# Optimization experiments

Measured on AMD Instinct MI355X. Metric: run time of the kernel, lower is better.

Reference implementation:

```python
import jax, jax.numpy as jnp
import numpy as np

B, DIM, N = 64, 128, 4000
H = 4
DH = DIM // H          # 32
CL = 50                # clusters (hardcoded in module)
K = 9                  # knn_num
SCALOR = DH ** -0.5


def setup_inputs() -> dict:
    key = jax.random.key(0)
    ks = jax.random.split(key, 16)
    s = 0.05
    inp = {
        'x': jax.random.normal(ks[0], (B, DIM, N, 1), jnp.float32),
        # conv_group1 / conv_group2: InstanceNorm(no affine) -> BN(affine) -> ReLU -> 1x1 conv
        'wg1': jax.random.normal(ks[1], (CL, DIM), jnp.float32) * s,
        'bg1': jnp.zeros((CL,), jnp.float32),
        'g1_gamma': jnp.ones((DIM,), jnp.float32),
        'g1_beta': jnp.zeros((DIM,), jnp.float32),
        'wg2': jax.random.normal(ks[2], (CL, DIM), jnp.float32) * s,
        'bg2': jnp.zeros((CL,), jnp.float32),
        'g2_gamma': jnp.ones((DIM,), jnp.float32),
        'g2_beta': jnp.zeros((DIM,), jnp.float32),
        # per-head 1x1 convs (stacked over heads)
        'qkv_w': jax.random.normal(ks[3], (H, DH, DIM), jnp.float32) * s,
        'qkv_b': jnp.zeros((H, DH), jnp.float32),
        'qkv1_w': jax.random.normal(ks[4], (H, 3 * DH, DIM), jnp.float32) * s,
        'qkv1_b': jnp.zeros((H, 3 * DH), jnp.float32),
        # GCBlock convs: conv1 (1,3) stride (1,3): 2*DH->DH ; conv2 (1,3): DH->DH
        'gc1_w': jax.random.normal(ks[5], (H, DH, 2 * DH, 3), jnp.float32) * s,
        'gc1_b': jnp.zeros((H, DH), jnp.float32),
        'gc1_gamma': jnp.ones((H, DH), jnp.float32),
        'gc1_beta': jnp.zeros((H, DH), jnp.float32),
        'gc2_w': jax.random.normal(ks[6], (H, DH, DH, 3), jnp.float32) * s,
        'gc2_b': jnp.zeros((H, DH), jnp.float32),
        'gc2_gamma': jnp.ones((H, DH), jnp.float32),
        'gc2_beta': jnp.zeros((H, DH), jnp.float32),
        # output projections
        'pres_w': jax.random.normal(ks[7], (DIM, 2 * DIM), jnp.float32) * s,
        'pres_b': jnp.zeros((DIM,), jnp.float32),
        'proj_w': jax.random.normal(ks[8], (DIM, DIM), jnp.float32) * s,
        'proj_b': jnp.zeros((DIM,), jnp.float32),
    }
    return inp


def _conv_group(x3, w, bconv, gamma, beta):
    # x3: (b, C, n). InstanceNorm2d(eps=1e-3, no affine) over n, BN(train) over (b,n), ReLU, 1x1 conv.
    mu = x3.mean(-1, keepdims=True)
    var = x3.var(-1, keepdims=True)
    xin = (x3 - mu) * jax.lax.rsqrt(var + 1e-3)
    mu2 = xin.mean((0, 2), keepdims=True)
    var2 = xin.var((0, 2), keepdims=True)
    xbn = gamma[None, :, None] * (xin - mu2) * jax.lax.rsqrt(var2 + 1e-5) + beta[None, :, None]
    xr = jax.nn.relu(xbn)
    return jnp.einsum('oc,bcn->bon', w, xr) + bconv[None, :, None]


def _bn_train(h, gamma, beta, axes):
    mu = h.mean(axes, keepdims=True)
    var = h.var(axes, keepdims=True)
    return gamma * (h - mu) * jax.lax.rsqrt(var + 1e-5) + beta


def _forward(x, wg1, bg1, g1_gamma, g1_beta, wg2, bg2, g2_gamma, g2_beta,
             qkv_w, qkv_b, qkv1_w, qkv1_b,
             gc1_w, gc1_b, gc1_gamma, gc1_beta,
             gc2_w, gc2_b, gc2_gamma, gc2_beta,
             pres_w, pres_b, proj_w, proj_b):
    xs = x[..., 0]                                          # (b, dim, n)
    # cluster assignment 1: softmax over points
    embed1 = _conv_group(xs, wg1, bg1, g1_gamma, g1_beta)   # (b, 50, n)
    S1 = jax.nn.softmax(embed1, axis=2)
    cluster_x = jnp.einsum('bdn,bcn->bdc', xs, S1)          # (b, dim, 50)

    # ---- local branch (per head, vectorized): 1x1 conv -> knn graph feature -> conv stack ----
    q = jnp.einsum('hod,bdc->bhoc', qkv_w, cluster_x) + qkv_b[None, :, :, None]  # (b,H,dh,50)
    xt = q.transpose(0, 1, 3, 2)                            # (b,H,50,dh)
    inner = jnp.einsum('bhnc,bhmc->bhnm', xt, xt)
    sq = jnp.sum(xt * xt, axis=-1)
    pd = 2.0 * inner - sq[..., :, None] - sq[..., None, :]  # negative squared distance
    idx = jax.lax.top_k(pd, K)[1]                            # (b,H,50,K)
    x_exp = jnp.broadcast_to(xt[:, :, None, :, :], xt.shape[:2] + (CL, CL, DH))
    feature = jnp.take_along_axis(x_exp, idx[..., None], axis=3)        # (b,H,50,K,dh)
    center = jnp.broadcast_to(xt[:, :, :, None, :], feature.shape)
    edge = jnp.concatenate([center, center - feature], axis=-1)          # (b,H,50,K,2dh)
    # conv1: kernel (1,3) stride (1,3): K=9 -> 3 windows of 3
    e = edge.reshape(edge.shape[0], H, CL, 3, 3, 2 * DH)
    h1 = jnp.einsum('bhnjti,hoit->bhnjo', e, gc1_w) + gc1_b[None, :, None, None, :]
    h1 = jax.nn.relu(_bn_train(h1, gc1_gamma[None, :, None, None, :], gc1_beta[None, :, None, None, :], (0, 2, 3)))
    # conv2: kernel (1,3): 3 -> 1
    h2 = jnp.einsum('bhnti,hoit->bhno', h1, gc2_w) + gc2_b[None, :, None, :]
    h2 = jax.nn.relu(_bn_train(h2, gc2_gamma[None, :, None, :], gc2_beta[None, :, None, :], (0, 2)))
    local = h2.transpose(0, 1, 3, 2)                        # (b,H,dh,50)

    # ---- global branch: tiny attention over 50 clusters per head ----
    qkv = jnp.einsum('hod,bdc->bhoc', qkv1_w, cluster_x) + qkv1_b[None, :, :, None]  # (b,H,3dh,50)
    qg, kg, vg = jnp.split(qkv, 3, axis=2)
    attn = jax.nn.softmax(SCALOR * jnp.einsum('bhdn,bhdm->bhnm', qg, kg), axis=-1)
    glob = jnp.einsum('bhnm,bhdm->bhdn', attn, vg)          # (b,H,dh,50)

    # interleave [local_h, global_h] per head along channels -> (b, 2*dim, 50)
    per_head = jnp.concatenate([local, glob], axis=2)       # (b,H,2dh,50)
    cat = per_head.reshape(per_head.shape[0], 2 * DIM, CL)
    res = jnp.einsum('oc,bcn->bon', pres_w, cat) + pres_b[None, :, None]  # (b,dim,50)

    # cluster assignment 2: softmax over clusters, scatter back to points
    embed2 = _conv_group(xs, wg2, bg2, g2_gamma, g2_beta)   # (b,50,n)
    S2 = jax.nn.softmax(embed2, axis=1)
    res2 = jnp.einsum('bdc,bcn->bdn', res, S2)              # (b,dim,n)
    out = jnp.einsum('od,bdn->bon', proj_w, res2) + proj_b[None, :, None]
    return out[..., None]                                   # (b,dim,n,1)


def reference(x, wg1, bg1, g1_gamma, g1_beta, wg2, bg2, g2_gamma, g2_beta,
              qkv_w, qkv_b, qkv1_w, qkv1_b,
              gc1_w, gc1_b, gc1_gamma, gc1_beta,
              gc2_w, gc2_b, gc2_gamma, gc2_beta,
              pres_w, pres_b, proj_w, proj_b):
    return _forward(x, wg1, bg1, g1_gamma, g1_beta, wg2, bg2, g2_gamma, g2_beta,
                    qkv_w, qkv_b, qkv1_w, qkv1_b,
                    gc1_w, gc1_b, gc1_gamma, gc1_beta,
                    gc2_w, gc2_b, gc2_gamma, gc2_beta,
                    pres_w, pres_b, proj_w, proj_b)
```

## Files before the change

### kernel.cpp

```cpp
#include <hip/hip_runtime.h>
#include <cstddef>


constexpr size_t O_MU    = 0;
constexpr size_t O_RINV  = 8192;
constexpr size_t O_RATIO = 16384;
constexpr size_t O_A1    = 24576;
constexpr size_t O_B1    = 24704;
constexpr size_t O_A2    = 24832;
constexpr size_t O_B2    = 24960;
constexpr size_t O_PROJWT= 25088;
constexpr size_t O_VPROJ = 41472;
constexpr size_t O_MT    = 41600;
constexpr size_t O_E2    = 74368;
constexpr size_t O_UCXP  = 12874368;
constexpr size_t O_CX    = 16659072;
constexpr size_t O_XT    = 17068672;
constexpr size_t O_QT    = 17478272;
constexpr size_t O_KT    = 17887872;
constexpr size_t O_VT    = 18297472;
constexpr size_t O_H1    = 18707072;
constexpr size_t O_P1    = 19935872;
constexpr size_t O_BN1S  = 19952256;
constexpr size_t O_BN1T  = 19952384;
constexpr size_t O_H2    = 19952512;
constexpr size_t O_P2    = 20362112;
constexpr size_t O_BN2S  = 20378496;
constexpr size_t O_BN2T  = 20378624;
constexpr size_t O_CAT   = 20378752;
constexpr size_t O_PRES2 = 21197952;

__global__ __launch_bounds__(256) void k_rowstats(const float* __restrict__ x,
                                                  float* __restrict__ ws){
  int row = blockIdx.x;
  const float4* xr = (const float4*)(x + (size_t)row * 4000);
  float s = 0.f, sq = 0.f;
  for(int i = threadIdx.x; i < 1000; i += 256){
    float4 v = xr[i];
    s  += v.x + v.y + v.z + v.w;
    sq += v.x*v.x + v.y*v.y + v.z*v.z + v.w*v.w;
  }
  __shared__ float ls[256], lq[256];
  ls[threadIdx.x] = s; lq[threadIdx.x] = sq; __syncthreads();
  for(int st = 128; st > 0; st >>= 1){
    if(threadIdx.x < st){ ls[threadIdx.x] += ls[threadIdx.x+st]; lq[threadIdx.x] += lq[threadIdx.x+st]; }
    __syncthreads();
  }
  if(threadIdx.x == 0){
    float mean = ls[0] * (1.f/4000.f);
    float var  = lq[0] * (1.f/4000.f) - mean*mean;
    ws[O_MU   + row] = mean;
    ws[O_RINV + row] = rsqrtf(var + 1e-3f);
    ws[O_RATIO+ row] = var / (var + 1e-3f);
  }
}

__global__ void k_prep(const float* g1g, const float* g1b,
                       const float* g2g, const float* g2b,
                       const float* presb, const float* projw,
                       float* __restrict__ ws){
  int t = threadIdx.x;
  if(t < 128){
    float s = 0.f;
    for(int b = 0; b < 64; b++) s += ws[O_RATIO + b*128 + t];
    float var2 = s * (1.f/64.f);
    float inv2 = rsqrtf(var2 + 1e-5f);
    ws[O_A1+t] = g1g[t] * inv2;  ws[O_B1+t] = g1b[t];
    ws[O_A2+t] = g2g[t] * inv2;  ws[O_B2+t] = g2b[t];
  }
  for(int i = t; i < 16384; i += 256){ int o = i & 127, k = i >> 7; ws[O_PROJWT+i] = projw[o*128 + k]; }
  __syncthreads();
  if(t < 128){
    float v = 0.f;
    for(int d = 0; d < 128; d++) v += ws[O_PROJWT + d*128 + t] * presb[d];
    ws[O_VPROJ + t] = v;
  }
}

__global__ __launch_bounds__(256) void k_mprep(const float* __restrict__ presw,
                                               float* __restrict__ ws){
  int kk2 = blockIdx.x * 2;
  __shared__ float pwc[2][128];
  int t = threadIdx.x;
  { int which = t >> 7, d = t & 127; pwc[which][d] = presw[d*256 + kk2 + which]; }
  __syncthreads();
  int which = t >> 7, o = t & 127;
  float acc = 0.f;
  for(int d = 0; d < 128; d++) acc += ws[O_PROJWT + d*128 + o] * pwc[which][d];
  ws[O_MT + (size_t)(kk2 + which)*128 + o] = acc;
}

__global__ __launch_bounds__(256) void k_fused(const float* __restrict__ x,
    const float* __restrict__ wg1, const float* __restrict__ bg1,
    const float* __restrict__ wg2, const float* __restrict__ bg2,
    float* __restrict__ ws){
  int ch = blockIdx.x, b = blockIdx.y;
  __shared__ float lW1[128*56];
  __shared__ float lW2[128*56];
  __shared__ float lrv1[128*64];
  __shared__ float lrv2[128*64];
  __shared__ float lxt [64*132];
  __shared__ float ca1[128], cb1[128], ca2[128], cb2[128];
  __shared__ float bg1p[64], bg2p[64];
  int t = threadIdx.x;
  if(t < 128){
    float mu = ws[O_MU + b*128 + t], ri = ws[O_RINV + b*128 + t];
    float a1 = ws[O_A1+t]*ri, a2 = ws[O_A2+t]*ri;
    ca1[t] = a1; cb1[t] = ws[O_B1+t] - a1*mu;
    ca2[t] = a2; cb2[t] = ws[O_B2+t] - a2*mu;
  }
  if(t < 64){ bg1p[t] = (t < 50) ? bg1[t] : 0.f; bg2p[t] = (t < 50) ? bg2[t] : 0.f; }
  for(int i = t; i < 1600; i += 256){
    int cl = i >> 5, cq = i & 31;
    float4 w1 = *(const float4*)&wg1[cl*128 + cq*4];
    float4 w2 = *(const float4*)&wg2[cl*128 + cq*4];
    int c0 = cq*4;
    lW1[(c0+0)*56+cl] = w1.x; lW1[(c0+1)*56+cl] = w1.y; lW1[(c0+2)*56+cl] = w1.z; lW1[(c0+3)*56+cl] = w1.w;
    lW2[(c0+0)*56+cl] = w2.x; lW2[(c0+1)*56+cl] = w2.y; lW2[(c0+2)*56+cl] = w2.z; lW2[(c0+3)*56+cl] = w2.w;
  }
  for(int i = t; i < 768; i += 256){
    int cl = 50 + i/128, c = i%128;
    lW1[c*56+cl] = 0.f; lW2[c*56+cl] = 0.f;
  }
  int dg = t % 33, cg = t / 33;
  float ua[4][8];
  #pragma unroll
  for(int r = 0; r < 4; r++)
    #pragma unroll
    for(int i = 0; i < 8; i++) ua[r][i] = 0.f;
  int ig = t >> 4, jg = t & 15;
  int clb = ig*4, j4 = jg*4;
  float e[4][4];

  for(int st = 0; st < 8; st++){
    int nb = ch*500 + st*64;
    int lim = (st == 7) ? 52 : 64;
    __syncthreads();
    for(int i = t; i < 2048; i += 256){
      int c = i >> 4, jj = (i & 15)*4;
      float4 xv = make_float4(0.f,0.f,0.f,0.f);
      if(jj < lim) xv = *(const float4*)&x[(size_t)(b*128 + c)*4000 + nb + jj];
      lxt[(jj+0)*132 + c] = xv.x; lxt[(jj+1)*132 + c] = xv.y;
      lxt[(jj+2)*132 + c] = xv.z; lxt[(jj+3)*132 + c] = xv.w;
      float a1 = ca1[c], b1v = cb1[c], a2 = ca2[c], b2v = cb2[c];
      float4 r1, r2;
      r1.x = fmaxf(a1*xv.x + b1v, 0.f); r1.y = fmaxf(a1*xv.y + b1v, 0.f);
      r1.z = fmaxf(a1*xv.z + b1v, 0.f); r1.w = fmaxf(a1*xv.w + b1v, 0.f);
      r2.x = fmaxf(a2*xv.x + b2v, 0.f); r2.y = fmaxf(a2*xv.y + b2v, 0.f);
      r2.z = fmaxf(a2*xv.z + b2v, 0.f); r2.w = fmaxf(a2*xv.w + b2v, 0.f);
      *(float4*)&lrv1[c*64 + jj] = r1;
      *(float4*)&lrv2[c*64 + jj] = r2;
    }
    if(t < 64){
      lxt[t*132 + 128] = (t < lim) ? 1.f : 0.f;
      lxt[t*132 + 129] = 0.f; lxt[t*132 + 130] = 0.f; lxt[t*132 + 131] = 0.f;
    }
    __syncthreads();
    if(ig < 14){
      #pragma unroll
      for(int r = 0; r < 4; r++){ e[r][0]=0.f; e[r][1]=0.f; e[r][2]=0.f; e[r][3]=0.f; }
      #pragma unroll 4
      for(int c = 0; c < 128; c++){
        float4 w = *(const float4*)&lW1[c*56 + clb];
        float4 v = *(const float4*)&lrv1[c*64 + j4];
        e[0][0] += w.x*v.x; e[0][1] += w.x*v.y; e[0][2] += w.x*v.z; e[0][3] += w.x*v.w;
        e[1][0] += w.y*v.x; e[1][1] += w.y*v.y; e[1][2] += w.y*v.z; e[1][3] += w.y*v.w;
        e[2][0] += w.z*v.x; e[2][1] += w.z*v.y; e[2][2] += w.z*v.z; e[2][3] += w.z*v.w;
        e[3][0] += w.w*v.x; e[3][1] += w.w*v.y; e[3][2] += w.w*v.z; e[3][3] += w.w*v.w;
      }
    }
    __syncthreads();
    if(ig < 14){
      #pragma unroll
      for(int r = 0; r < 4; r++){
        float bias = bg1p[clb + r];
        float4 u;
        u.x = expf(e[r][0] + bias); u.y = expf(e[r][1] + bias);
        u.z = expf(e[r][2] + bias); u.w = expf(e[r][3] + bias);
        *(float4*)&lrv1[(clb + r)*64 + j4] = u;
      }
    }
    __syncthreads();
    if(t < 231){
      int d4 = dg*4, cb8 = cg*8;
      #pragma unroll 2
      for(int n = 0; n < 64; n++){
        float4 xv = *(const float4*)&lxt[n*132 + d4];
        #pragma unroll
        for(int i = 0; i < 8; i++){
          float u = lrv1[(cb8 + i)*64 + n];
          ua[0][i] += xv.x*u; ua[1][i] += xv.y*u;
          ua[2][i] += xv.z*u; ua[3][i] += xv.w*u;
        }
      }
    }
    if(ig < 14){
      #pragma unroll
      for(int r = 0; r < 4; r++){ e[r][0]=0.f; e[r][1]=0.f; e[r][2]=0.f; e[r][3]=0.f; }
      #pragma unroll 4
      for(int c = 0; c < 128; c++){
        float4 w = *(const float4*)&lW2[c*56 + clb];
        float4 v = *(const float4*)&lrv2[c*64 + j4];
        e[0][0] += w.x*v.x; e[0][1] += w.x*v.y; e[0][2] += w.x*v.z; e[0][3] += w.x*v.w;
        e[1][0] += w.y*v.x; e[1][1] += w.y*v.y; e[1][2] += w.y*v.z; e[1][3] += w.y*v.w;
        e[2][0] += w.z*v.x; e[2][1] += w.z*v.y; e[2][2] += w.z*v.z; e[2][3] += w.z*v.w;
        e[3][0] += w.w*v.x; e[3][1] += w.w*v.y; e[3][2] += w.w*v.z; e[3][3] += w.w*v.w;
      }
      if(j4 < lim){
        #pragma unroll
        for(int r = 0; r < 4; r++){
          int cl = clb + r;
          if(cl < 50){
            float bias = bg2p[cl];
            float4 o = make_float4(e[r][0]+bias, e[r][1]+bias, e[r][2]+bias, e[r][3]+bias);
            *(float4*)&ws[O_E2 + ((size_t)b*50 + cl)*4000 + nb + j4] = o;
          }
        }
      }
    }
  }
  if(t < 231){
    int d4 = dg*4, cb8 = cg*8;
    #pragma unroll
    for(int r = 0; r < 4; r++){
      size_t base = O_UCXP + ((size_t)(ch*64 + b)*132 + d4 + r)*56 + cb8;
      *(float4*)&ws[base]     = make_float4(ua[r][0], ua[r][1], ua[r][2], ua[r][3]);
      *(float4*)&ws[base + 4] = make_float4(ua[r][4], ua[r][5], ua[r][6], ua[r][7]);
    }
  }
}

__global__ __launch_bounds__(256) void k_cxred(float* __restrict__ ws){
  int b = blockIdx.x, t = threadIdx.x;
  __shared__ float zi[64];
  if(t < 50){
    float s = 0.f;
    for(int ch = 0; ch < 8; ch++)
      s += ws[O_UCXP + ((size_t)(ch*64 + b)*132 + 128)*56 + t];
    zi[t] = 1.f / s;
  }
  __syncthreads();
  for(int i = t; i < 6400; i += 256){
    int d = i / 50, c = i % 50;
    float s = 0.f;
    for(int ch = 0; ch < 8; ch++)
      s += ws[O_UCXP + ((size_t)(ch*64 + b)*132 + d)*56 + c];
    ws[O_CX + (size_t)b*6400 + d*50 + c] = s * zi[c];
  }
}

__global__ __launch_bounds__(256) void k_qkv(const float* __restrict__ qw,
                                             const float* __restrict__ qb,
                                             const float* __restrict__ q1w,
                                             const float* __restrict__ q1b,
                                             float* __restrict__ ws){
  int rt = blockIdx.x, b = blockIdx.y;
  __shared__ float wl[64*130];
  __shared__ float cxl[128*52];
  int t = threadIdx.x;
  for(int i = t; i < 2048; i += 256){
    int rl = i >> 5, kq = i & 31, row = rt*64 + rl;
    float4 w = (row < 128) ? *(const float4*)&qw[row*128 + kq*4]
                           : *(const float4*)&q1w[(row-128)*128 + kq*4];
    int k0 = kq*4;
    wl[rl*130 + k0+0] = w.x; wl[rl*130 + k0+1] = w.y;
    wl[rl*130 + k0+2] = w.z; wl[rl*130 + k0+3] = w.w;
  }
  for(int i = t; i < 6656; i += 256){
    int k = i / 52, c = i % 52;
    cxl[i] = (c < 50) ? ws[O_CX + (size_t)b*6400 + k*50 + c] : 0.f;
  }
  __syncthreads();
  int ig = t & 15, cg = t >> 4;
  float acc[4][4];
  #pragma unroll
  for(int r = 0; r < 4; r++){ acc[r][0]=0.f; acc[r][1]=0.f; acc[r][2]=0.f; acc[r][3]=0.f; }
  if(cg < 13){
    int rb = ig*4, cb = cg*4;
    #pragma unroll 4
    for(int k = 0; k < 128; k++){
      float4 cv = *(const float4*)&cxl[k*52 + cb];
      float w0 = wl[(rb+0)*130 + k], w1 = wl[(rb+1)*130 + k];
      float w2 = wl[(rb+2)*130 + k], w3 = wl[(rb+3)*130 + k];
      acc[0][0] += w0*cv.x; acc[0][1] += w0*cv.y; acc[0][2] += w0*cv.z; acc[0][3] += w0*cv.w;
      acc[1][0] += w1*cv.x; acc[1][1] += w1*cv.y; acc[1][2] += w1*cv.z; acc[1][3] += w1*cv.w;
      acc[2][0] += w2*cv.x; acc[2][1] += w2*cv.y; acc[2][2] += w2*cv.z; acc[2][3] += w2*cv.w;
      acc[3][0] += w3*cv.x; acc[3][1] += w3*cv.y; acc[3][2] += w3*cv.z; acc[3][3] += w3*cv.w;
    }
    #pragma unroll
    for(int r = 0; r < 4; r++){
      int row = rt*64 + ig*4 + r;
      size_t base; float bias;
      if(row < 128){
        int h = row >> 5;
        bias = qb[row];
        base = O_XT + (size_t)(b*4 + h)*1600 + (row & 31);
      }else{
        int r2 = row - 128, h = r2/96, j = r2%96, kind = j >> 5, dd = j & 31;
        bias = q1b[r2];
        base = (kind==0 ? O_QT : kind==1 ? O_KT : O_VT) + (size_t)(b*4 + h)*1600 + dd;
      }
      #pragma unroll
      for(int s = 0; s < 4; s++){
        int c = cg*4 + s;
        if(c < 50) ws[base + (size_t)c*32] = acc[r][s] + bias;
      }
    }
  }
}

__global__ __launch_bounds__(256) void k_knn(const float* __restrict__ g1w,
                                             const float* __restrict__ g1bias,
                                             float* __restrict__ ws){
  int h = blockIdx.x, b = blockIdx.y;
  __shared__ float xtl[50][33];
  __shared__ float pdl[50][52];
  __shared__ float sql[50];
  __shared__ int   idxl[50][9];
  __shared__ float w1l[6144];
  int t = threadIdx.x;
  const float* xtg = ws + O_XT + (size_t)(b*4 + h)*1600;
  for(int i = t; i < 1600; i += 256) xtl[i >> 5][i & 31] = xtg[i];
  for(int i = t; i < 6144; i += 256){
    int o = i / 192, r = i % 192, ii = r / 3, tt = r % 3;
    w1l[(ii*3 + tt)*32 + o] = g1w[(size_t)h*6144 + i];
  }
  __syncthreads();
  if(t < 50){
    float s = 0.f;
    for(int d = 0; d < 32; d++){ float v = xtl[t][d]; s += v*v; }
    sql[t] = s;
  }
  __syncthreads();
  for(int i = t; i < 2500; i += 256){
    int n = i / 50, m = i % 50;
    float s = 0.f;
    for(int d = 0; d < 32; d++) s += xtl[n][d]*xtl[m][d];
    pdl[n][m] = 2.f*s - sql[n] - sql[m];
  }
  __syncthreads();
  if(t < 50){
    float pv = INFINITY; int pi = -1;
    for(int k = 0; k < 9; k++){
      float bv = -INFINITY; int bi = 1000;
      for(int m = 0; m < 50; m++){
        float v = pdl[t][m];
        bool elig = (v < pv) || (v == pv && m > pi);
        if(elig && (v > bv || (v == bv && m < bi))){ bv = v; bi = m; }
      }
      idxl[t][k] = bi; pv = bv; pi = bi;
    }
  }
  __syncthreads();
  if(t < 150){
    int n = t / 3, jw = t % 3;
    float acc[32];
    #pragma unroll
    for(int o = 0; o < 32; o++) acc[o] = 0.f;
    for(int t3 = 0; t3 < 3; t3++){
      int kx = idxl[n][jw*3 + t3];
      for(int ii = 0; ii < 32; ii++){
        float c0 = xtl[n][ii];
        float c1 = c0 - xtl[kx][ii];
        const float* wr0 = w1l + (ii*3 + t3)*32;
        const float* wr1 = w1l + ((ii+32)*3 + t3)*32;
        #pragma unroll
        for(int o = 0; o < 32; o++) acc[o] += c0*wr0[o] + c1*wr1[o];
      }
    }
    float* out = ws + O_H1 + ((size_t)(b*4 + h)*150 + n*3 + jw)*32;
    #pragma unroll
    for(int o = 0; o < 32; o++) out[o] = acc[o] + g1bias[h*32 + o];
  }
}

__global__ void k_bn1p(float* __restrict__ ws){
  int b = blockIdx.x, t = threadIdx.x;
  int p = t & 127, half = t >> 7;
  int h = p >> 5, o = p & 31;
  const float* src = ws + O_H1 + (size_t)b*19200;
  float s = 0.f, sq = 0.f;
  for(int nj = half*75; nj < half*75 + 75; nj++){
    float v = src[(h*150 + nj)*32 + o];
    s += v; sq += v*v;
  }
  __shared__ float ls[256], lq[256];
  ls[t] = s; lq[t] = sq; __syncthreads();
  if(t < 128){
    ws[O_P1 + b*256 + p]       = ls[t] + ls[t+128];
    ws[O_P1 + b*256 + 128 + p] = lq[t] + lq[t+128];
  }
}

__global__ void k_bn1f(const float* g, const float* be, float* __restrict__ ws){
  int t = threadIdx.x;
  if(t < 128){
    float s = 0.f, sq = 0.f;
    for(int b = 0; b < 64; b++){ s += ws[O_P1 + b*256 + t]; sq += ws[O_P1 + b*256 + 128 + t]; }
    float mean = s * (1.f/9600.f), var = sq * (1.f/9600.f) - mean*mean;
    float sc = g[t] * rsqrtf(var + 1e-5f);
    ws[O_BN1S+t] = sc; ws[O_BN1T+t] = be[t] - sc*mean;
  }
}

__global__ __launch_bounds__(256) void k_conv2(const float* __restrict__ g2w,
                                               const float* __restrict__ g2bias,
                                               float* __restrict__ ws){
  int h = blockIdx.x, b = blockIdx.y;
  __shared__ float hl[150][33];
  __shared__ float w2l[3072];
  __shared__ float rs[8][32], rq[8][32];
  int t = threadIdx.x;
  const float* h1p = ws + O_H1 + (size_t)(b*4 + h)*4800;
  for(int i = t; i < 4800; i += 256){
    int nj = i >> 5, ii = i & 31;
    hl[nj][ii] = fmaxf(ws[O_BN1S + h*32 + ii]*h1p[i] + ws[O_BN1T + h*32 + ii], 0.f);
  }
  for(int i = t; i < 3072; i += 256){
    int o = i / 96, r = i % 96, ii = r / 3, tt = r % 3;
    w2l[(ii*3 + tt)*32 + o] = g2w[(size_t)h*3072 + i];
  }
  __syncthreads();
  int o = t & 31, ng = t >> 5;
  float bias = g2bias[h*32 + o];
  float s = 0.f, sq = 0.f;
  for(int n = ng; n < 50; n += 8){
    float acc = 0.f;
    for(int t3 = 0; t3 < 3; t3++){
      const float* hr = hl[n*3 + t3];
      #pragma unroll
      for(int ii = 0; ii < 32; ii++) acc += hr[ii] * w2l[(ii*3 + t3)*32 + o];
    }
    acc += bias;
    ws[O_H2 + ((size_t)(b*4 + h)*50 + n)*32 + o] = acc;
    s += acc; sq += acc*acc;
  }
  rs[ng][o] = s; rq[ng][o] = sq; __syncthreads();
  if(t < 32){
    float S = 0.f, Q = 0.f;
    for(int g2 = 0; g2 < 8; g2++){ S += rs[g2][t]; Q += rq[g2][t]; }
    ws[O_P2 + (b*4 + h)*64 + t]      = S;
    ws[O_P2 + (b*4 + h)*64 + 32 + t] = Q;
  }
}

__global__ void k_bn2f(const float* g, const float* be, float* __restrict__ ws){
  int t = threadIdx.x;
  if(t < 128){
    int h = t >> 5, o = t & 31;
    float s = 0.f, sq = 0.f;
    for(int b = 0; b < 64; b++){
      s  += ws[O_P2 + (size_t)(b*4 + h)*64 + o];
      sq += ws[O_P2 + (size_t)(b*4 + h)*64 + 32 + o];
    }
    float mean = s * (1.f/3200.f), var = sq * (1.f/3200.f) - mean*mean;
    float sc = g[t] * rsqrtf(var + 1e-5f);
    ws[O_BN2S+t] = sc; ws[O_BN2T+t] = be[t] - sc*mean;
  }
}

__global__ __launch_bounds__(256) void k_attn(float* __restrict__ ws){
  int h = blockIdx.x, b = blockIdx.y;
  __shared__ float qtl[50][33], ktl[50][33], vtl[50][33], al[50][52];
  int t = threadIdx.x;
  size_t base = (size_t)(b*4 + h)*1600;
  for(int i = t; i < 1600; i += 256){
    int n = i >> 5, d = i & 31;
    qtl[n][d] = ws[O_QT + base + i];
    ktl[n][d] = ws[O_KT + base + i];
    vtl[n][d] = ws[O_VT + base + i];
  }
  __syncthreads();
  for(int i = t; i < 2500; i += 256){
    int n = i / 50, m = i % 50;
    float s = 0.f;
    for(int d = 0; d < 32; d++) s += qtl[n][d]*ktl[m][d];
    al[n][m] = s * 0.17677669529663687f;
  }
  __syncthreads();
  if(t < 50){
    float m = -INFINITY;
    for(int j = 0; j < 50; j++) m = fmaxf(m, al[t][j]);
    float s = 0.f;
    for(int j = 0; j < 50; j++){ float e = expf(al[t][j] - m); al[t][j] = e; s += e; }
    float inv = 1.f/s;
    for(int j = 0; j < 50; j++) al[t][j] *= inv;
  }
  __syncthreads();
  for(int i = t; i < 1600; i += 256){
    int n = i >> 5, d = i & 31;
    float gacc = 0.f;
    for(int m = 0; m < 50; m++) gacc += al[n][m]*vtl[m][d];
    ws[O_CAT + ((size_t)b*256 + h*64 + 32 + d)*50 + n] = gacc;
    float l = fmaxf(ws[O_BN2S + h*32 + d]*ws[O_H2 + ((size_t)(b*4 + h)*50 + n)*32 + d] + ws[O_BN2T + h*32 + d], 0.f);
    ws[O_CAT + ((size_t)b*256 + h*64 + d)*50 + n] = l;
  }
}

__global__ __launch_bounds__(256) void k_res(float* __restrict__ ws){
  int b = blockIdx.x;
  __shared__ float mtl[64*132];
  __shared__ float catl[64*52];
  __shared__ float vp[128];
  int t = threadIdx.x;
  if(t < 128) vp[t] = ws[O_VPROJ + t];
  int og = t >> 4, cg = t & 15;
  int ob = og*8, cb = cg*4;
  float acc[8][4];
  #pragma unroll
  for(int r = 0; r < 8; r++){ acc[r][0]=0.f; acc[r][1]=0.f; acc[r][2]=0.f; acc[r][3]=0.f; }
  for(int kc = 0; kc < 4; kc++){
    int k0 = kc*64;
    __syncthreads();
    for(int i = t; i < 2048; i += 256){
      int k = i >> 5, oq = i & 31;
      float4 m = *(const float4*)&ws[O_MT + (size_t)(k0 + k)*128 + oq*4];
      *(float4*)&mtl[k*132 + oq*4] = m;
    }
    for(int i = t; i < 3328; i += 256){
      int k = i / 52, c = i % 52;
      catl[i] = (c < 50) ? ws[O_CAT + (size_t)b*12800 + (k0 + k)*50 + c] : 0.f;
    }
    __syncthreads();
    if(cg < 13){
      #pragma unroll 2
      for(int k = 0; k < 64; k++){
        float4 m0 = *(const float4*)&mtl[k*132 + ob];
        float4 m1 = *(const float4*)&mtl[k*132 + ob + 4];
        float4 cv = *(const float4*)&catl[k*52 + cb];
        acc[0][0] += m0.x*cv.x; acc[0][1] += m0.x*cv.y; acc[0][2] += m0.x*cv.z; acc[0][3] += m0.x*cv.w;
        acc[1][0] += m0.y*cv.x; acc[1][1] += m0.y*cv.y; acc[1][2] += m0.y*cv.z; acc[1][3] += m0.y*cv.w;
        acc[2][0] += m0.z*cv.x; acc[2][1] += m0.z*cv.y; acc[2][2] += m0.z*cv.z; acc[2][3] += m0.z*cv.w;
        acc[3][0] += m0.w*cv.x; acc[3][1] += m0.w*cv.y; acc[3][2] += m0.w*cv.z; acc[3][3] += m0.w*cv.w;
        acc[4][0] += m1.x*cv.x; acc[4][1] += m1.x*cv.y; acc[4][2] += m1.x*cv.z; acc[4][3] += m1.x*cv.w;
        acc[5][0] += m1.y*cv.x; acc[5][1] += m1.y*cv.y; acc[5][2] += m1.y*cv.z; acc[5][3] += m1.y*cv.w;
        acc[6][0] += m1.z*cv.x; acc[6][1] += m1.z*cv.y; acc[6][2] += m1.z*cv.z; acc[6][3] += m1.z*cv.w;
        acc[7][0] += m1.w*cv.x; acc[7][1] += m1.w*cv.y; acc[7][2] += m1.w*cv.z; acc[7][3] += m1.w*cv.w;
      }
    }
  }
  if(cg < 13){
    #pragma unroll
    for(int s = 0; s < 4; s++){
      int c = cb + s;
      if(c < 50){
        float4 o0 = make_float4(acc[0][s]+vp[ob+0], acc[1][s]+vp[ob+1], acc[2][s]+vp[ob+2], acc[3][s]+vp[ob+3]);
        float4 o1 = make_float4(acc[4][s]+vp[ob+4], acc[5][s]+vp[ob+5], acc[6][s]+vp[ob+6], acc[7][s]+vp[ob+7]);
        *(float4*)&ws[O_PRES2 + (size_t)b*6400 + c*128 + ob]     = o0;
        *(float4*)&ws[O_PRES2 + (size_t)b*6400 + c*128 + ob + 4] = o1;
      }
    }
  }
}

__global__ __launch_bounds__(256) void k_out(const float* __restrict__ projb,
                                             float* __restrict__ ws,
                                             float* __restrict__ out){
  int nt = blockIdx.x, b = blockIdx.y;
  int n0 = nt*64;
  __shared__ float sl[50*64];
  __shared__ float p2l[50*132];
  __shared__ float pb[128];
  int t = threadIdx.x;
  for(int i = t; i < 3200; i += 256){
    int c = i >> 6, j = i & 63, n = n0 + j;
    sl[i] = (n < 4000) ? ws[O_E2 + ((size_t)b*50 + c)*4000 + n] : 0.f;
  }
  for(int i = t; i < 6400; i += 256){
    int c = i >> 7, o = i & 127;
    p2l[c*132 + o] = ws[O_PRES2 + (size_t)b*6400 + c*128 + o];
  }
  if(t < 128) pb[t] = projb[t];
  __syncthreads();
  if(t < 64){
    int j = t;
    float m = -INFINITY;
    for(int c = 0; c < 50; c++) m = fmaxf(m, sl[c*64 + j]);
    float s = 0.f;
    for(int c = 0; c < 50; c++){ float e = expf(sl[c*64 + j] - m); sl[c*64 + j] = e; s += e; }
    float inv = 1.f/s;
    for(int c = 0; c < 50; c++) sl[c*64 + j] *= inv;
  }
  __syncthreads();
  int og = t >> 4, jg = t & 15;
  int ob = og*8, j4 = jg*4;
  float acc[8][4];
  #pragma unroll
  for(int r = 0; r < 8; r++){ acc[r][0]=0.f; acc[r][1]=0.f; acc[r][2]=0.f; acc[r][3]=0.f; }
  #pragma unroll 2
  for(int c = 0; c < 50; c++){
    float4 sv = *(const float4*)&sl[c*64 + j4];
    float4 p0 = *(const float4*)&p2l[c*132 + ob];
    float4 p1 = *(const float4*)&p2l[c*132 + ob + 4];
    acc[0][0] += p0.x*sv.x; acc[0][1] += p0.x*sv.y; acc[0][2] += p0.x*sv.z; acc[0][3] += p0.x*sv.w;
    acc[1][0] += p0.y*sv.x; acc[1][1] += p0.y*sv.y; acc[1][2] += p0.y*sv.z; acc[1][3] += p0.y*sv.w;
    acc[2][0] += p0.z*sv.x; acc[2][1] += p0.z*sv.y; acc[2][2] += p0.z*sv.z; acc[2][3] += p0.z*sv.w;
    acc[3][0] += p0.w*sv.x; acc[3][1] += p0.w*sv.y; acc[3][2] += p0.w*sv.z; acc[3][3] += p0.w*sv.w;
    acc[4][0] += p1.x*sv.x; acc[4][1] += p1.x*sv.y; acc[4][2] += p1.x*sv.z; acc[4][3] += p1.x*sv.w;
    acc[5][0] += p1.y*sv.x; acc[5][1] += p1.y*sv.y; acc[5][2] += p1.y*sv.z; acc[5][3] += p1.y*sv.w;
    acc[6][0] += p1.z*sv.x; acc[6][1] += p1.z*sv.y; acc[6][2] += p1.z*sv.z; acc[6][3] += p1.z*sv.w;
    acc[7][0] += p1.w*sv.x; acc[7][1] += p1.w*sv.y; acc[7][2] += p1.w*sv.z; acc[7][3] += p1.w*sv.w;
  }
  int n = n0 + j4;
  if(n < 4000){
    #pragma unroll
    for(int r = 0; r < 8; r++){
      float bv = pb[ob + r];
      float4 o = make_float4(acc[r][0]+bv, acc[r][1]+bv, acc[r][2]+bv, acc[r][3]+bv);
      *(float4*)&out[(size_t)(b*128 + ob + r)*4000 + n] = o;
    }
  }
}

extern "C" void kernel_launch(void* const* d_in, const int* in_sizes, int n_in,
                              void* d_out, int out_size, void* d_ws, size_t ws_size,
                              hipStream_t stream){
  (void)in_sizes; (void)n_in; (void)out_size; (void)ws_size;
  const float* x      = (const float*)d_in[0];
  const float* wg1    = (const float*)d_in[1];
  const float* bg1    = (const float*)d_in[2];
  const float* g1g    = (const float*)d_in[3];
  const float* g1b    = (const float*)d_in[4];
  const float* wg2    = (const float*)d_in[5];
  const float* bg2    = (const float*)d_in[6];
  const float* g2g    = (const float*)d_in[7];
  const float* g2b    = (const float*)d_in[8];
  const float* qkvw   = (const float*)d_in[9];
  const float* qkvb   = (const float*)d_in[10];
  const float* qkv1w  = (const float*)d_in[11];
  const float* qkv1b  = (const float*)d_in[12];
  const float* gc1w   = (const float*)d_in[13];
  const float* gc1bias= (const float*)d_in[14];
  const float* gc1g   = (const float*)d_in[15];
  const float* gc1be  = (const float*)d_in[16];
  const float* gc2w   = (const float*)d_in[17];
  const float* gc2bias= (const float*)d_in[18];
  const float* gc2g   = (const float*)d_in[19];
  const float* gc2be  = (const float*)d_in[20];
  const float* presw  = (const float*)d_in[21];
  const float* presb  = (const float*)d_in[22];
  const float* projw  = (const float*)d_in[23];
  const float* projb  = (const float*)d_in[24];
  float* ws = (float*)d_ws;
  float* out = (float*)d_out;

  k_rowstats<<<8192, 256, 0, stream>>>(x, ws);
  k_prep<<<1, 256, 0, stream>>>(g1g, g1b, g2g, g2b, presb, projw, ws);
  k_mprep<<<128, 256, 0, stream>>>(presw, ws);
  k_fused<<<dim3(8, 64), 256, 0, stream>>>(x, wg1, bg1, wg2, bg2, ws);
  k_cxred<<<64, 256, 0, stream>>>(ws);
  k_qkv<<<dim3(8, 64), 256, 0, stream>>>(qkvw, qkvb, qkv1w, qkv1b, ws);
  k_knn<<<dim3(4, 64), 256, 0, stream>>>(gc1w, gc1bias, ws);
  k_bn1p<<<64, 256, 0, stream>>>(ws);
  k_bn1f<<<1, 128, 0, stream>>>(gc1g, gc1be, ws);
  k_conv2<<<dim3(4, 64), 256, 0, stream>>>(gc2w, gc2bias, ws);
  k_bn2f<<<1, 128, 0, stream>>>(gc2g, gc2be, ws);
  k_attn<<<dim3(4, 64), 256, 0, stream>>>(ws);
  k_res<<<64, 256, 0, stream>>>(ws);
  k_out<<<dim3(63, 64), 256, 0, stream>>>(projb, ws, out);
}
```

Baseline: 865.6 us.

## Split fused cluster-embedding kernel into separate E1/UCX and E2 kernels

Splits the single fused kernel, which computed both cluster embeddings and the x·u accumulation, into two kernels. Each now uses far less shared memory, so more blocks can be resident per CU. The E1 kernel uses 48-point tiles and computes the softmax normaliser with an explicit row sum instead of the constant-one column trick. It also reorganises the accumulation loop with float4 loads of u. The cost is reading x twice from global memory and one extra kernel launch.

```diff
diff --git a/kernel.cpp b/kernel.cpp
--- a/kernel.cpp
+++ b/kernel.cpp
@@ -90,48 +90,172 @@
   ws[O_MT + (size_t)(kk2 + which)*128 + o] = acc;
 }
 
-__global__ __launch_bounds__(256) void k_fused(const float* __restrict__ x,
+__global__ __launch_bounds__(256) void k_e1ucx(const float* __restrict__ x,
     const float* __restrict__ wg1, const float* __restrict__ bg1,
-    const float* __restrict__ wg2, const float* __restrict__ bg2,
     float* __restrict__ ws){
   int ch = blockIdx.x, b = blockIdx.y;
-  __shared__ float lW1[128*56];
-  __shared__ float lW2[128*56];
-  __shared__ float lrv1[128*64];
-  __shared__ float lrv2[128*64];
-  __shared__ float lxt [64*132];
-  __shared__ float ca1[128], cb1[128], ca2[128], cb2[128];
-  __shared__ float bg1p[64], bg2p[64];
+  __shared__ float lW1[128*52];
+  __shared__ float lrv1[128*48];
+  __shared__ float lxt [48*132];
+  __shared__ float ca1[128], cb1[128];
+  __shared__ float bg1p[56];
   int t = threadIdx.x;
   if(t < 128){
     float mu = ws[O_MU + b*128 + t], ri = ws[O_RINV + b*128 + t];
-    float a1 = ws[O_A1+t]*ri, a2 = ws[O_A2+t]*ri;
+    float a1 = ws[O_A1+t]*ri;
     ca1[t] = a1; cb1[t] = ws[O_B1+t] - a1*mu;
-    ca2[t] = a2; cb2[t] = ws[O_B2+t] - a2*mu;
-  }
-  if(t < 64){ bg1p[t] = (t < 50) ? bg1[t] : 0.f; bg2p[t] = (t < 50) ? bg2[t] : 0.f; }
-  for(int i = t; i < 1600; i += 256){
+  }
+  if(t < 56) bg1p[t] = (t < 50) ? bg1[t] : 0.f;
+  for(int i = t; i < 1664; i += 256){
     int cl = i >> 5, cq = i & 31;
-    float4 w1 = *(const float4*)&wg1[cl*128 + cq*4];
-    float4 w2 = *(const float4*)&wg2[cl*128 + cq*4];
+    float4 w = (cl < 50) ? *(const float4*)&wg1[cl*128 + cq*4] : make_float4(0.f,0.f,0.f,0.f);
     int c0 = cq*4;
-    lW1[(c0+0)*56+cl] = w1.x; lW1[(c0+1)*56+cl] = w1.y; lW1[(c0+2)*56+cl] = w1.z; lW1[(c0+3)*56+cl] = w1.w;
-    lW2[(c0+0)*56+cl] = w2.x; lW2[(c0+1)*56+cl] = w2.y; lW2[(c0+2)*56+cl] = w2.z; lW2[(c0+3)*56+cl] = w2.w;
-  }
-  for(int i = t; i < 768; i += 256){
-    int cl = 50 + i/128, c = i%128;
-    lW1[c*56+cl] = 0.f; lW2[c*56+cl] = 0.f;
-  }
-  int dg = t % 33, cg = t / 33;
+    lW1[(c0+0)*52+cl] = w.x; lW1[(c0+1)*52+cl] = w.y;
+    lW1[(c0+2)*52+cl] = w.z; lW1[(c0+3)*52+cl] = w.w;
+  }
+  int dg = t & 31, cg = t >> 5;
   float ua[4][8];
   #pragma unroll
   for(int r = 0; r < 4; r++)
     #pragma unroll
     for(int i = 0; i < 8; i++) ua[r][i] = 0.f;
+  float zacc = 0.f;
   int ig = t >> 4, jg = t & 15;
   int clb = ig*4, j4 = jg*4;
-  float e[4][4];
-
+
+  for(int st = 0; st < 11; st++){
+    int nb = ch*500 + st*48;
+    int lim = (st == 10) ? 20 : 48;
+    __syncthreads();
+    for(int i = t; i < 1536; i += 256){
+      int c = i / 12, jj = (i % 12)*4;
+      float4 xv = make_float4(0.f,0.f,0.f,0.f);
+      if(jj < lim) xv = *(const float4*)&x[(size_t)(b*128 + c)*4000 + nb + jj];
+      lxt[(jj+0)*132 + c] = xv.x; lxt[(jj+1)*132 + c] = xv.y;
+      lxt[(jj+2)*132 + c] = xv.z; lxt[(jj+3)*132 + c] = xv.w;
+      float a1 = ca1[c], b1v = cb1[c];
+      float4 r1;
+      r1.x = fmaxf(a1*xv.x + b1v, 0.f); r1.y = fmaxf(a1*xv.y + b1v, 0.f);
+      r1.z = fmaxf(a1*xv.z + b1v, 0.f); r1.w = fmaxf(a1*xv.w + b1v, 0.f);
+      *(float4*)&lrv1[c*48 + jj] = r1;
+    }
+    __syncthreads();
+    float e[4][4];
+    if(ig < 13 && jg < 12){
+      #pragma unroll
+      for(int r = 0; r < 4; r++){ e[r][0]=0.f; e[r][1]=0.f; e[r][2]=0.f; e[r][3]=0.f; }
+      #pragma unroll 4
+      for(int c = 0; c < 128; c++){
+        float4 w = *(const float4*)&lW1[c*52 + clb];
+        float4 v = *(const float4*)&lrv1[c*48 + j4];
+        e[0][0] += w.x*v.x; e[0][1] += w.x*v.y; e[0][2] += w.x*v.z; e[0][3] += w.x*v.w;
+        e[1][0] += w.y*v.x; e[1][1] += w.y*v.y; e[1][2] += w.y*v.z; e[1][3] += w.y*v.w;
+        e[2][0] += w.z*v.x; e[2][1] += w.z*v.y; e[2][2] += w.z*v.z; e[2][3] += w.z*v.w;
+        e[3][0] += w.w*v.x; e[3][1] += w.w*v.y; e[3][2] += w.w*v.z; e[3][3] += w.w*v.w;
+      }
+    }
+    __syncthreads();
+    if(ig < 13 && jg < 12){
+      bool live = (j4 < lim);
+      #pragma unroll
+      for(int r = 0; r < 4; r++){
+        float bias = bg1p[clb + r];
+        float4 u = make_float4(0.f,0.f,0.f,0.f);
+        if(live){
+          u.x = expf(e[r][0] + bias); u.y = expf(e[r][1] + bias);
+          u.z = expf(e[r][2] + bias); u.w = expf(e[r][3] + bias);
+        }
+        *(float4*)&lrv1[(clb + r)*48 + j4] = u;
+      }
+    }
+    __syncthreads();
+    if(t < 224){
+      int d4 = dg*4, c8 = cg*8;
+      for(int n4 = 0; n4 < 12; n4++){
+        int n0 = n4*4;
+        float4 uv[8];
+        #pragma unroll
+        for(int i = 0; i < 8; i++) uv[i] = *(const float4*)&lrv1[(c8 + i)*48 + n0];
+        {
+          float4 xq = *(const float4*)&lxt[(n0+0)*132 + d4];
+          #pragma unroll
+          for(int i = 0; i < 8; i++){
+            float u = uv[i].x;
+            ua[0][i] += xq.x*u; ua[1][i] += xq.y*u; ua[2][i] += xq.z*u; ua[3][i] += xq.w*u;
+          }
+        }
+        {
+          float4 xq = *(const float4*)&lxt[(n0+1)*132 + d4];
+          #pragma unroll
+          for(int i = 0; i < 8; i++){
+            float u = uv[i].y;
+            ua[0][i] += xq.x*u; ua[1][i] += xq.y*u; ua[2][i] += xq.z*u; ua[3][i] += xq.w*u;
+          }
+        }
+        {
+          float4 xq = *(const float4*)&lxt[(n0+2)*132 + d4];
+          #pragma unroll
+          for(int i = 0; i < 8; i++){
+            float u = uv[i].z;
+            ua[0][i] += xq.x*u; ua[1][i] += xq.y*u; ua[2][i] += xq.z*u; ua[3][i] += xq.w*u;
+          }
+        }
+        {
+          float4 xq = *(const float4*)&lxt[(n0+3)*132 + d4];
+          #pragma unroll
+          for(int i = 0; i < 8; i++){
+            float u = uv[i].w;
+            ua[0][i] += xq.x*u; ua[1][i] += xq.y*u; ua[2][i] += xq.z*u; ua[3][i] += xq.w*u;
+          }
+        }
+      }
+    }
+    if(t < 52){
+      float s = 0.f;
+      #pragma unroll
+      for(int k = 0; k < 12; k++){
+        float4 u = *(const float4*)&lrv1[t*48 + k*4];
+        s += u.x + u.y + u.z + u.w;
+      }
+      zacc += s;
+    }
+  }
+  if(t < 224){
+    int d4 = dg*4, c8 = cg*8;
+    #pragma unroll
+    for(int r = 0; r < 4; r++){
+      size_t base = O_UCXP + ((size_t)(ch*64 + b)*132 + d4 + r)*56 + c8;
+      *(float4*)&ws[base]     = make_float4(ua[r][0], ua[r][1], ua[r][2], ua[r][3]);
+      *(float4*)&ws[base + 4] = make_float4(ua[r][4], ua[r][5], ua[r][6], ua[r][7]);
+    }
+  }
+  if(t < 52) ws[O_UCXP + ((size_t)(ch*64 + b)*132 + 128)*56 + t] = zacc;
+}
+
+__global__ __launch_bounds__(256) void k_e2(const float* __restrict__ x,
+    const float* __restrict__ wg2, const float* __restrict__ bg2,
+    float* __restrict__ ws){
+  int ch = blockIdx.x, b = blockIdx.y;
+  __shared__ float lW2[128*52];
+  __shared__ float lrv2[128*64];
+  __shared__ float ca2[128], cb2[128];
+  __shared__ float bg2p[56];
+  int t = threadIdx.x;
+  if(t < 128){
+    float mu = ws[O_MU + b*128 + t], ri = ws[O_RINV + b*128 + t];
+    float a2 = ws[O_A2+t]*ri;
+    ca2[t] = a2; cb2[t] = ws[O_B2+t] - a2*mu;
+  }
+  if(t < 56) bg2p[t] = (t < 50) ? bg2[t] : 0.f;
+  for(int i = t; i < 1664; i += 256){
+    int cl = i >> 5, cq = i & 31;
+    float4 w = (cl < 50) ? *(const float4*)&wg2[cl*128 + cq*4] : make_float4(0.f,0.f,0.f,0.f);
+    int c0 = cq*4;
+    lW2[(c0+0)*52+cl] = w.x; lW2[(c0+1)*52+cl] = w.y;
+    lW2[(c0+2)*52+cl] = w.z; lW2[(c0+3)*52+cl] = w.w;
+  }
+  int ig = t >> 4, jg = t & 15;
+  int clb = ig*4, j4 = jg*4;
   for(int st = 0; st < 8; st++){
     int nb = ch*500 + st*64;
     int lim = (st == 7) ? 52 : 64;
@@ -140,66 +264,20 @@
       int c = i >> 4, jj = (i & 15)*4;
       float4 xv = make_float4(0.f,0.f,0.f,0.f);
       if(jj < lim) xv = *(const float4*)&x[(size_t)(b*128 + c)*4000 + nb + jj];
-      lxt[(jj+0)*132 + c] = xv.x; lxt[(jj+1)*132 + c] = xv.y;
-      lxt[(jj+2)*132 + c] = xv.z; lxt[(jj+3)*132 + c] = xv.w;
-      float a1 = ca1[c], b1v = cb1[c], a2 = ca2[c], b2v = cb2[c];
-      float4 r1, r2;
-      r1.x = fmaxf(a1*xv.x + b1v, 0.f); r1.y = fmaxf(a1*xv.y + b1v, 0.f);
-      r1.z = fmaxf(a1*xv.z + b1v, 0.f); r1.w = fmaxf(a1*xv.w + b1v, 0.f);
+      float a2 = ca2[c], b2v = cb2[c];
+      float4 r2;
       r2.x = fmaxf(a2*xv.x + b2v, 0.f); r2.y = fmaxf(a2*xv.y + b2v, 0.f);
       r2.z = fmaxf(a2*xv.z + b2v, 0.f); r2.w = fmaxf(a2*xv.w + b2v, 0.f);
-      *(float4*)&lrv1[c*64 + jj] = r1;
       *(float4*)&lrv2[c*64 + jj] = r2;
     }
-    if(t < 64){
-      lxt[t*132 + 128] = (t < lim) ? 1.f : 0.f;
-      lxt[t*132 + 129] = 0.f; lxt[t*132 + 130] = 0.f; lxt[t*132 + 131] = 0.f;
-    }
-    __syncthreads();
-    if(ig < 14){
+    __syncthreads();
+    if(ig < 13){
+      float e[4][4];
       #pragma unroll
       for(int r = 0; r < 4; r++){ e[r][0]=0.f; e[r][1]=0.f; e[r][2]=0.f; e[r][3]=0.f; }
       #pragma unroll 4
       for(int c = 0; c < 128; c++){
-        float4 w = *(const float4*)&lW1[c*56 + clb];
-        float4 v = *(const float4*)&lrv1[c*64 + j4];
-        e[0][0] += w.x*v.x; e[0][1] += w.x*v.y; e[0][2] += w.x*v.z; e[0][3] += w.x*v.w;
-        e[1][0] += w.y*v.x; e[1][1] += w.y*v.y; e[1][2] += w.y*v.z; e[1][3] += w.y*v.w;
-        e[2][0] += w.z*v.x; e[2][1] += w.z*v.y; e[2][2] += w.z*v.z; e[2][3] += w.z*v.w;
-        e[3][0] += w.w*v.x; e[3][1] += w.w*v.y; e[3][2] += w.w*v.z; e[3][3] += w.w*v.w;
-      }
-    }
-    __syncthreads();
-    if(ig < 14){
-      #pragma unroll
-      for(int r = 0; r < 4; r++){
-        float bias = bg1p[clb + r];
-        float4 u;
-        u.x = expf(e[r][0] + bias); u.y = expf(e[r][1] + bias);
-        u.z = expf(e[r][2] + bias); u.w = expf(e[r][3] + bias);
-        *(float4*)&lrv1[(clb + r)*64 + j4] = u;
-      }
-    }
-    __syncthreads();
-    if(t < 231){
-      int d4 = dg*4, cb8 = cg*8;
-      #pragma unroll 2
-      for(int n = 0; n < 64; n++){
-        float4 xv = *(const float4*)&lxt[n*132 + d4];
-        #pragma unroll
-        for(int i = 0; i < 8; i++){
-          float u = lrv1[(cb8 + i)*64 + n];
-          ua[0][i] += xv.x*u; ua[1][i] += xv.y*u;
-          ua[2][i] += xv.z*u; ua[3][i] += xv.w*u;
-        }
-      }
-    }
-    if(ig < 14){
-      #pragma unroll
-      for(int r = 0; r < 4; r++){ e[r][0]=0.f; e[r][1]=0.f; e[r][2]=0.f; e[r][3]=0.f; }
-      #pragma unroll 4
-      for(int c = 0; c < 128; c++){
-        float4 w = *(const float4*)&lW2[c*56 + clb];
+        float4 w = *(const float4*)&lW2[c*52 + clb];
         float4 v = *(const float4*)&lrv2[c*64 + j4];
         e[0][0] += w.x*v.x; e[0][1] += w.x*v.y; e[0][2] += w.x*v.z; e[0][3] += w.x*v.w;
         e[1][0] += w.y*v.x; e[1][1] += w.y*v.y; e[1][2] += w.y*v.z; e[1][3] += w.y*v.w;
@@ -217,15 +295,6 @@
           }
         }
       }
-    }
-  }
-  if(t < 231){
-    int d4 = dg*4, cb8 = cg*8;
-    #pragma unroll
-    for(int r = 0; r < 4; r++){
-      size_t base = O_UCXP + ((size_t)(ch*64 + b)*132 + d4 + r)*56 + cb8;
-      *(float4*)&ws[base]     = make_float4(ua[r][0], ua[r][1], ua[r][2], ua[r][3]);
-      *(float4*)&ws[base + 4] = make_float4(ua[r][4], ua[r][5], ua[r][6], ua[r][7]);
     }
   }
 }
@@ -647,7 +716,8 @@
   k_rowstats<<<8192, 256, 0, stream>>>(x, ws);
   k_prep<<<1, 256, 0, stream>>>(g1g, g1b, g2g, g2b, presb, projw, ws);
   k_mprep<<<128, 256, 0, stream>>>(presw, ws);
-  k_fused<<<dim3(8, 64), 256, 0, stream>>>(x, wg1, bg1, wg2, bg2, ws);
+  k_e1ucx<<<dim3(8, 64), 256, 0, stream>>>(x, wg1, bg1, ws);
+  k_e2<<<dim3(8, 64), 256, 0, stream>>>(x, wg2, bg2, ws);
   k_cxred<<<64, 256, 0, stream>>>(ws);
   k_qkv<<<dim3(8, 64), 256, 0, stream>>>(qkvw, qkvb, qkv1w, qkv1b, ws);
   k_knn<<<dim3(4, 64), 256, 0, stream>>>(gc1w, gc1bias, ws);
```

Result: faster. 796.8 us (-7.9%).
